# Optimization experiments

Hardware: AMD Instinct MI355X
Metric: run time of the kernel (lower is better)

## Reference

```python
import jax, jax.numpy as jnp
import numpy as np

BETA = 0.3        # SmoothL1Loss beta
LAMBDA_PHY = 0.15 # physics loss weight


def smooth_l1(d, beta):
    ad = jnp.abs(d)
    return jnp.where(ad < beta, 0.5 * d * d / beta, ad - 0.5 * beta)


def setup_inputs() -> dict:
    key = jax.random.key(0)
    k1, k2, k3, k4 = jax.random.split(key, 4)
    B, Z = 16384, 2048
    preds = jax.random.normal(k1, (B, Z, 1), dtype=jnp.float32)
    targets = jax.random.normal(k2, (B, Z), dtype=jnp.float32)
    current_temps = jax.random.normal(k3, (B, Z), dtype=jnp.float32)
    adjacency = jax.random.randint(k4, (Z, Z), 0, 2).astype(jnp.int32)
    return {"preds": preds, "targets": targets,
            "current_temps": current_temps, "adjacency": adjacency}


def reference(preds, targets, current_temps, adjacency):
    p = preds[:, :, 0]                               # [B, Z]
    num_zones = p.shape[1]
    pred_loss = smooth_l1(p - targets, BETA).mean()
    pred_change = p - current_temps                  # [B, Z]

    # Vectorized neighbor mean: replaces the per-zone Python loop with one
    # dense masked-adjacency contraction.
    mask = (adjacency > 0).astype(p.dtype)           # [Z, Z]
    deg = mask.sum(axis=1)                           # [Z]
    has_nb = deg > 0
    safe_deg = jnp.where(has_nb, deg, 1.0)
    avg_neighbor = jnp.einsum('zn,bn->bz', mask, current_temps) / safe_deg  # [B, Z]

    temp_diff = current_temps - avg_neighbor         # [B, Z]
    violation = jax.nn.softplus(temp_diff * pred_change)
    per_zone = violation.mean(axis=0)                # mean over batch, [Z]
    physics_loss = jnp.where(has_nb, per_zone, 0.0).sum() / num_zones

    total_loss = pred_loss + LAMBDA_PHY * physics_loss
    return (total_loss, physics_loss)
```

## Files before the change

kernel.cpp:

```cpp
#include <hip/hip_runtime.h>
#include <hip/hip_bf16.h>
#include <cmath>

#define BETA 0.3f
#define LAMBDA_PHY 0.15f

#define BM 128
#define BN 128
#define BKE 128
#define NT 256

typedef float f32x4 __attribute__((ext_vector_type(4)));
typedef int   i32x4 __attribute__((ext_vector_type(4)));
typedef int   i32x8 __attribute__((ext_vector_type(8)));

#define AS1 __attribute__((address_space(1)))
#define AS3 __attribute__((address_space(3)))

#define FENCE() asm volatile("" ::: "memory")
#define BARRIER() do { FENCE(); __builtin_amdgcn_s_barrier(); FENCE(); } while (0)
#define WAITV8() asm volatile("s_waitcnt vmcnt(8)" ::: "memory")
#define WAITV0() asm volatile("s_waitcnt vmcnt(0)" ::: "memory")

__device__ __forceinline__ float softplus_f(float x) {
    return fmaxf(x, 0.0f) + __logf(1.0f + __expf(-fabsf(x)));
}

__device__ __forceinline__ float smooth_l1_f(float d) {
    float ad = fabsf(d);
    return (ad < BETA) ? (0.5f / BETA) * d * d : (ad - 0.5f * BETA);
}

__device__ __forceinline__ unsigned f_e4m3(float f) {
    unsigned u = __builtin_bit_cast(unsigned, f);
    unsigned s = (u >> 24) & 0x80u;
    unsigned ab = u & 0x7fffffffu;
    float a = __builtin_bit_cast(float, ab);
    if (a >= 448.f) return s | 0x7Eu;
    if (a < 0.015625f) {
        int q = (int)rintf(a * 512.f);
        return s | (unsigned)q;
    }
    unsigned r = ab + 0x7FFFFu + ((ab >> 20) & 1u);
    unsigned ee = (r >> 23) - 120u;
    unsigned m = (r >> 20) & 7u;
    return s | (ee << 3) | m;
}

__global__ void k_prepconv(const int* __restrict__ adj, unsigned char* __restrict__ maskf8,
                           float* __restrict__ invdeg, float* __restrict__ hasnb, int Z,
                           const float* __restrict__ src, uint4* __restrict__ dst,
                           long n16, int ncb) {
    int t = threadIdx.x;
    if ((int)blockIdx.x < Z) {
        int z = blockIdx.x;
        const int* row = adj + (size_t)z * Z;
        unsigned char* mrow = maskf8 + (size_t)z * Z;
        int cnt = 0;
        for (int n = t; n < Z; n += blockDim.x) {
            int a = (row[n] > 0);
            mrow[n] = a ? (unsigned char)0x38 : (unsigned char)0;
            cnt += a;
        }
        for (int o = 32; o; o >>= 1) cnt += __shfl_down(cnt, o);
        __shared__ int rs[4];
        int lane = t & 63, wave = t >> 6;
        if (lane == 0) rs[wave] = cnt;
        __syncthreads();
        if (t == 0) {
            int deg = rs[0] + rs[1] + rs[2] + rs[3];
            invdeg[z] = (deg > 0) ? 1.0f / (float)deg : 1.0f;
            hasnb[z]  = (deg > 0) ? 1.0f : 0.0f;
        }
    } else {
        long i = (long)(blockIdx.x - Z) * blockDim.x + t;
        long stride = (long)ncb * blockDim.x;
        for (; i < n16; i += stride) {
            const float4* s = (const float4*)(src + i * 16);
            uint4 o;
            unsigned w[4];
#pragma unroll
            for (int q = 0; q < 4; ++q) {
                float4 v = s[q];
                w[q] = f_e4m3(v.x) | (f_e4m3(v.y) << 8) | (f_e4m3(v.z) << 16) | (f_e4m3(v.w) << 24);
            }
            o.x = w[0]; o.y = w[1]; o.z = w[2]; o.w = w[3];
            dst[i] = o;
        }
    }
}

__global__ __launch_bounds__(NT, 2) void k_gemm(
    const unsigned char* __restrict__ Af8,
    const unsigned char* __restrict__ Bf8,
    const float* __restrict__ preds,
    const float* __restrict__ targets,
    const float* __restrict__ ctemps,
    const float* __restrict__ invdeg,
    const float* __restrict__ hasnb,
    float* __restrict__ partials,
    int M, int N, int K)
{
    __shared__ __align__(16) unsigned char AsF[2 * BM * BKE];
    __shared__ __align__(16) unsigned char BsF[2 * BN * BKE];

    const int nwg = gridDim.x;
    const int ob = blockIdx.x;
    const int bid = (nwg % 8 == 0) ? ((ob % 8) * (nwg / 8) + ob / 8) : ob;
    const int ntiles = N / BN;
    const int mt = bid / ntiles;
    const int nt = bid % ntiles;
    const int row0 = mt * BM;
    const int col0 = nt * BN;
    const int t = threadIdx.x;
    const int lane = t & 63;
    const int wave = t >> 6;
    const int wm = wave >> 1;
    const int wn = wave & 1;
    const int fr = lane & 15;
    const int fq = lane >> 4;
    const int fr7 = fr & 7;

    const int tr = t >> 3;
    const int tc = t & 7;
    const int cs = tc ^ (tr & 7);

    int ofsA[2], ofsB[2];
#pragma unroll
    for (int p = 0; p < 2; ++p) {
        const int sp = (((fq + 4 * p) ^ fr7) << 4);
        ofsA[p] = (wm * 64 + fr) * BKE + sp;
        ofsB[p] = (wn * 64 + fr) * BKE + sp;
    }

    f32x4 acc[4][4];
#pragma unroll
    for (int m = 0; m < 4; ++m)
#pragma unroll
        for (int n = 0; n < 4; ++n)
            acc[m][n] = (f32x4){0.f, 0.f, 0.f, 0.f};

    const unsigned char* aSrc = Af8 + (size_t)(row0 + tr) * K + cs * 16;
    const unsigned char* bSrc = Bf8 + (size_t)(col0 + tr) * K + cs * 16;
    unsigned char* aDstC = &AsF[t * 16];
    unsigned char* bDstC = &BsF[t * 16];

#define STAGE(BUF) do {                                                                      \
    _Pragma("unroll")                                                                        \
    for (int r_ = 0; r_ < 4; ++r_)                                                           \
        __builtin_amdgcn_global_load_lds((const AS1 void*)(aSrc + (size_t)(r_ * 32) * K),    \
                                         (AS3 void*)(aDstC + (BUF) * 16384 + r_ * 4096), 16, 0, 0); \
    _Pragma("unroll")                                                                        \
    for (int r_ = 0; r_ < 4; ++r_)                                                           \
        __builtin_amdgcn_global_load_lds((const AS1 void*)(bSrc + (size_t)(r_ * 32) * K),    \
                                         (AS3 void*)(bDstC + (BUF) * 16384 + r_ * 4096), 16, 0, 0); \
    aSrc += BKE; bSrc += BKE;                                                                \
} while (0)

#define MFMA_TILE(BUF) do {                                                                  \
    i32x8 af_[4], bv_[4];                                                                    \
    _Pragma("unroll")                                                                        \
    for (int mi_ = 0; mi_ < 4; ++mi_) {                                                      \
        i32x4 lo_ = *(const i32x4*)(AsF + (BUF) * 16384 + ofsA[0] + mi_ * 2048);             \
        i32x4 hi_ = *(const i32x4*)(AsF + (BUF) * 16384 + ofsA[1] + mi_ * 2048);             \
        af_[mi_] = (i32x8){lo_[0], lo_[1], lo_[2], lo_[3], hi_[0], hi_[1], hi_[2], hi_[3]};  \
    }                                                                                        \
    _Pragma("unroll")                                                                        \
    for (int ni_ = 0; ni_ < 4; ++ni_) {                                                      \
        i32x4 lo_ = *(const i32x4*)(BsF + (BUF) * 16384 + ofsB[0] + ni_ * 2048);             \
        i32x4 hi_ = *(const i32x4*)(BsF + (BUF) * 16384 + ofsB[1] + ni_ * 2048);             \
        bv_[ni_] = (i32x8){lo_[0], lo_[1], lo_[2], lo_[3], hi_[0], hi_[1], hi_[2], hi_[3]};  \
    }                                                                                        \
    __builtin_amdgcn_s_setprio(1);                                                           \
    _Pragma("unroll")                                                                        \
    for (int mi_ = 0; mi_ < 4; ++mi_)                                                        \
    _Pragma("unroll")                                                                        \
    for (int ni_ = 0; ni_ < 4; ++ni_)                                                        \
        acc[mi_][ni_] = __builtin_amdgcn_mfma_scale_f32_16x16x128_f8f6f4(                    \
            af_[mi_], bv_[ni_], acc[mi_][ni_], 0, 0, 0, 0x7F, 0, 0x7F);                      \
    __builtin_amdgcn_s_setprio(0);                                                           \
} while (0)

    const int nk = K / BKE;
    const int nk2 = nk >> 1;
    STAGE(0);

    for (int i = 0; i < nk2; ++i) {
        STAGE(1);
        WAITV8();
        BARRIER();
        MFMA_TILE(0);
        BARRIER();
        if (i + 1 < nk2) {
            STAGE(0);
            WAITV8();
        } else {
            WAITV0();
        }
        BARRIER();
        MFMA_TILE(1);
        BARRIER();
    }

#undef STAGE
#undef MFMA_TILE

    const size_t rbase = (size_t)(row0 + wm * 64 + fq * 4) * N;
    const float* pB = preds   + rbase;
    const float* tB = targets + rbase;
    const float* cB = ctemps  + rbase;

    float vsum = 0.f, ssum = 0.f;
#pragma unroll
    for (int n = 0; n < 4; ++n) {
        const int z = col0 + wn * 64 + n * 16 + fr;
        const float idg = invdeg[z];
        const float hnb = hasnb[z];
#pragma unroll
        for (int mb = 0; mb < 2; ++mb) {
            float pv[8], tv[8], cf[8];
#pragma unroll
            for (int m2 = 0; m2 < 2; ++m2)
#pragma unroll
                for (int j = 0; j < 4; ++j) {
                    const size_t o = (size_t)((mb * 2 + m2) * 16 + j) * N + z;
                    pv[m2 * 4 + j] = pB[o];
                    tv[m2 * 4 + j] = tB[o];
                    cf[m2 * 4 + j] = cB[o];
                }
#pragma unroll
            for (int m2 = 0; m2 < 2; ++m2)
#pragma unroll
                for (int j = 0; j < 4; ++j) {
                    const int q = m2 * 4 + j;
                    float avg = acc[mb * 2 + m2][n][j] * idg;
                    float c = cf[q];
                    float p = pv[q];
                    float x = (c - avg) * (p - c);
                    vsum += softplus_f(x) * hnb;
                    ssum += smooth_l1_f(p - tv[q]);
                }
        }
    }
    for (int o = 32; o; o >>= 1) { vsum += __shfl_down(vsum, o); ssum += __shfl_down(ssum, o); }
    __shared__ float rv[4], rsm[4];
    if (lane == 0) { rv[wave] = vsum; rsm[wave] = ssum; }
    __syncthreads();
    if (t == 0) {
        partials[2 * (size_t)ob]     = rv[0] + rv[1] + rv[2] + rv[3];
        partials[2 * (size_t)ob + 1] = rsm[0] + rsm[1] + rsm[2] + rsm[3];
    }
}

__global__ void k_finalize(const float* __restrict__ partials, int nblk,
                           float* __restrict__ out, float invBZ) {
    __shared__ float sv[256], ss[256];
    int t = threadIdx.x;
    float v = 0.f, s = 0.f;
    for (int i = t; i < nblk; i += 256) { v += partials[2 * (size_t)i]; s += partials[2 * (size_t)i + 1]; }
    sv[t] = v; ss[t] = s;
    __syncthreads();
    for (int o = 128; o; o >>= 1) {
        if (t < o) { sv[t] += sv[t + o]; ss[t] += ss[t + o]; }
        __syncthreads();
    }
    if (t == 0) {
        float phys = sv[0] * invBZ;
        float pred = ss[0] * invBZ;
        out[0] = pred + LAMBDA_PHY * phys;
        out[1] = phys;
    }
}

__global__ void k_zero2(float* p) { if (threadIdx.x < 2) p[threadIdx.x] = 0.f; }

__global__ void k_fallback(const float* __restrict__ preds, const float* __restrict__ targets,
                           const float* __restrict__ ctemps, const int* __restrict__ adj,
                           float* __restrict__ acc2, int B, int Z) {
    extern __shared__ float crow[];
    int nzb = (Z + 255) / 256;
    int b = blockIdx.x / nzb;
    int zb = blockIdx.x % nzb;
    int t = threadIdx.x;
    const float* cr = ctemps + (size_t)b * Z;
    for (int n = t; n < Z; n += 256) crow[n] = cr[n];
    __syncthreads();
    int z = zb * 256 + t;
    float vsum = 0.f, ssum = 0.f;
    if (z < Z) {
        const int* arow = adj + (size_t)z * Z;
        float sum = 0.f; int deg = 0;
        for (int n = 0; n < Z; ++n) {
            if (arow[n] > 0) { sum += crow[n]; ++deg; }
        }
        float avg = (deg > 0) ? sum / (float)deg : 0.f;
        float c = crow[z];
        size_t idx = (size_t)b * Z + z;
        float p = preds[idx];
        float x = (c - avg) * (p - c);
        vsum = (deg > 0) ? softplus_f(x) : 0.f;
        ssum = smooth_l1_f(p - targets[idx]);
    }
    for (int o = 32; o; o >>= 1) { vsum += __shfl_down(vsum, o); ssum += __shfl_down(ssum, o); }
    __shared__ float rv[4], rs2[4];
    int lane = t & 63, wave = t >> 6;
    if (lane == 0) { rv[wave] = vsum; rs2[wave] = ssum; }
    __syncthreads();
    if (t == 0) {
        atomicAdd(&acc2[0], rv[0] + rv[1] + rv[2] + rv[3]);
        atomicAdd(&acc2[1], rs2[0] + rs2[1] + rs2[2] + rs2[3]);
    }
}

extern "C" void kernel_launch(void* const* d_in, const int* in_sizes, int n_in,
                              void* d_out, int out_size, void* d_ws, size_t ws_size,
                              hipStream_t stream) {
    const float* preds   = (const float*)d_in[0];
    const float* targets = (const float*)d_in[1];
    const float* ctemps  = (const float*)d_in[2];
    const int*   adj     = (const int*)d_in[3];
    float* out = (float*)d_out;

    long zz = in_sizes[3];
    int Z = (int)llround(sqrt((double)zz));
    int B = in_sizes[1] / Z;

    size_t off = 0;
    size_t maskOff = off; off += (size_t)Z * Z;
    size_t cf8Off  = off; off += (size_t)B * Z;
    size_t idgOff  = off; off += (size_t)Z * 4;
    size_t hnbOff  = off; off += (size_t)Z * 4;
    int nblk = (Z > 0 && B > 0 && (B % BM) == 0 && (Z % BN) == 0) ? (B / BM) * (Z / BN) : 0;
    size_t partOff = off; off += (size_t)(nblk > 0 ? nblk : 1) * 2 * 4;

    bool main_ok = (B % BM == 0) && (Z % BN == 0) && (Z % BKE == 0) &&
                   (((Z / BKE) % 2) == 0) && ((B * Z) % 16 == 0) && (ws_size >= off);

    float invBZ = (float)(1.0 / ((double)B * (double)Z));

    if (main_ok) {
        char* ws = (char*)d_ws;
        unsigned char* maskf8 = (unsigned char*)(ws + maskOff);
        unsigned char* cf8    = (unsigned char*)(ws + cf8Off);
        float* idg      = (float*)(ws + idgOff);
        float* hnb      = (float*)(ws + hnbOff);
        float* partials = (float*)(ws + partOff);

        long n16 = (long)B * Z / 16;
        int ncb = 2048;
        k_prepconv<<<Z + ncb, 256, 0, stream>>>(adj, maskf8, idg, hnb, Z,
                                                ctemps, (uint4*)cf8, n16, ncb);
        k_gemm<<<nblk, NT, 0, stream>>>(cf8, maskf8, preds, targets, ctemps, idg, hnb,
                                        partials, B, Z, Z);
        k_finalize<<<1, 256, 0, stream>>>(partials, nblk, out, invBZ);
    } else {
        float* acc2 = (float*)d_ws;
        k_zero2<<<1, 64, 0, stream>>>(acc2);
        int nzb = (Z + 255) / 256;
        k_fallback<<<B * nzb, 256, (size_t)Z * 4, stream>>>(preds, targets, ctemps, adj, acc2, B, Z);
        k_finalize<<<1, 256, 0, stream>>>(acc2, 1, out, invBZ);
    }
}
```

Before: 186.9 us.

## Shrink GEMM N-tile to 64 and load B fragments directly from global

The GEMM tile width drops from 128 to 64 columns, and the B operand's LDS staging buffer is removed. Each wave now loads its B fragments straight from global memory into registers once per K-step, and launch bounds are raised so more blocks can fit per CU. The aim is to cut LDS footprint and B staging overhead and get more occupancy for latency hiding. The cost is that the large A matrix is re-read twice as often across column tiles, so arithmetic intensity per tile drops, and the B register loads are not coalesced through LDS.

```diff
diff --git a/kernel.cpp b/kernel.cpp
--- a/kernel.cpp
+++ b/kernel.cpp
@@ -6,7 +6,7 @@
 #define LAMBDA_PHY 0.15f
 
 #define BM 128
-#define BN 128
+#define BN 64
 #define BKE 128
 #define NT 256
 
@@ -90,7 +90,7 @@
     }
 }
 
-__global__ __launch_bounds__(NT, 2) void k_gemm(
+__global__ __launch_bounds__(NT, 4) void k_gemm(
     const unsigned char* __restrict__ Af8,
     const unsigned char* __restrict__ Bf8,
     const float* __restrict__ preds,
@@ -102,7 +102,6 @@
     int M, int N, int K)
 {
     __shared__ __align__(16) unsigned char AsF[2 * BM * BKE];
-    __shared__ __align__(16) unsigned char BsF[2 * BN * BKE];
 
     const int nwg = gridDim.x;
     const int ob = blockIdx.x;
@@ -125,59 +124,57 @@
     const int tc = t & 7;
     const int cs = tc ^ (tr & 7);
 
-    int ofsA[2], ofsB[2];
-#pragma unroll
-    for (int p = 0; p < 2; ++p) {
-        const int sp = (((fq + 4 * p) ^ fr7) << 4);
-        ofsA[p] = (wm * 64 + fr) * BKE + sp;
-        ofsB[p] = (wn * 64 + fr) * BKE + sp;
-    }
-
-    f32x4 acc[4][4];
+    int ofsA[2];
+#pragma unroll
+    for (int p = 0; p < 2; ++p)
+        ofsA[p] = (wm * 64 + fr) * BKE + (((fq + 4 * p) ^ fr7) << 4);
+
+    f32x4 acc[4][2];
 #pragma unroll
     for (int m = 0; m < 4; ++m)
 #pragma unroll
-        for (int n = 0; n < 4; ++n)
+        for (int n = 0; n < 2; ++n)
             acc[m][n] = (f32x4){0.f, 0.f, 0.f, 0.f};
 
     const unsigned char* aSrc = Af8 + (size_t)(row0 + tr) * K + cs * 16;
-    const unsigned char* bSrc = Bf8 + (size_t)(col0 + tr) * K + cs * 16;
+    const unsigned char* bP0 = Bf8 + (size_t)(col0 + wn * 32 + fr) * K + fq * 16;
+    const unsigned char* bP1 = bP0 + (size_t)16 * K;
     unsigned char* aDstC = &AsF[t * 16];
-    unsigned char* bDstC = &BsF[t * 16];
 
 #define STAGE(BUF) do {                                                                      \
     _Pragma("unroll")                                                                        \
     for (int r_ = 0; r_ < 4; ++r_)                                                           \
         __builtin_amdgcn_global_load_lds((const AS1 void*)(aSrc + (size_t)(r_ * 32) * K),    \
                                          (AS3 void*)(aDstC + (BUF) * 16384 + r_ * 4096), 16, 0, 0); \
-    _Pragma("unroll")                                                                        \
-    for (int r_ = 0; r_ < 4; ++r_)                                                           \
-        __builtin_amdgcn_global_load_lds((const AS1 void*)(bSrc + (size_t)(r_ * 32) * K),    \
-                                         (AS3 void*)(bDstC + (BUF) * 16384 + r_ * 4096), 16, 0, 0); \
-    aSrc += BKE; bSrc += BKE;                                                                \
+    aSrc += BKE;                                                                             \
 } while (0)
 
-#define MFMA_TILE(BUF) do {                                                                  \
-    i32x8 af_[4], bv_[4];                                                                    \
+#define LOADB(BV0, BV1) do {                                                                 \
+    i32x4 b0_ = *(const i32x4*)(bP0);                                                        \
+    i32x4 b1_ = *(const i32x4*)(bP0 + 64);                                                   \
+    i32x4 c0_ = *(const i32x4*)(bP1);                                                        \
+    i32x4 c1_ = *(const i32x4*)(bP1 + 64);                                                   \
+    BV0 = (i32x8){b0_[0], b0_[1], b0_[2], b0_[3], b1_[0], b1_[1], b1_[2], b1_[3]};           \
+    BV1 = (i32x8){c0_[0], c0_[1], c0_[2], c0_[3], c1_[0], c1_[1], c1_[2], c1_[3]};           \
+    bP0 += BKE; bP1 += BKE;                                                                  \
+} while (0)
+
+#define MFMA_TILE(BUF, BV0, BV1) do {                                                        \
+    i32x8 af_[4];                                                                            \
     _Pragma("unroll")                                                                        \
     for (int mi_ = 0; mi_ < 4; ++mi_) {                                                      \
         i32x4 lo_ = *(const i32x4*)(AsF + (BUF) * 16384 + ofsA[0] + mi_ * 2048);             \
         i32x4 hi_ = *(const i32x4*)(AsF + (BUF) * 16384 + ofsA[1] + mi_ * 2048);             \
         af_[mi_] = (i32x8){lo_[0], lo_[1], lo_[2], lo_[3], hi_[0], hi_[1], hi_[2], hi_[3]};  \
     }                                                                                        \
-    _Pragma("unroll")                                                                        \
-    for (int ni_ = 0; ni_ < 4; ++ni_) {                                                      \
-        i32x4 lo_ = *(const i32x4*)(BsF + (BUF) * 16384 + ofsB[0] + ni_ * 2048);             \
-        i32x4 hi_ = *(const i32x4*)(BsF + (BUF) * 16384 + ofsB[1] + ni_ * 2048);             \
-        bv_[ni_] = (i32x8){lo_[0], lo_[1], lo_[2], lo_[3], hi_[0], hi_[1], hi_[2], hi_[3]};  \
-    }                                                                                        \
     __builtin_amdgcn_s_setprio(1);                                                           \
     _Pragma("unroll")                                                                        \
-    for (int mi_ = 0; mi_ < 4; ++mi_)                                                        \
-    _Pragma("unroll")                                                                        \
-    for (int ni_ = 0; ni_ < 4; ++ni_)                                                        \
-        acc[mi_][ni_] = __builtin_amdgcn_mfma_scale_f32_16x16x128_f8f6f4(                    \
-            af_[mi_], bv_[ni_], acc[mi_][ni_], 0, 0, 0, 0x7F, 0, 0x7F);                      \
+    for (int mi_ = 0; mi_ < 4; ++mi_) {                                                      \
+        acc[mi_][0] = __builtin_amdgcn_mfma_scale_f32_16x16x128_f8f6f4(                      \
+            af_[mi_], BV0, acc[mi_][0], 0, 0, 0, 0x7F, 0, 0x7F);                             \
+        acc[mi_][1] = __builtin_amdgcn_mfma_scale_f32_16x16x128_f8f6f4(                      \
+            af_[mi_], BV1, acc[mi_][1], 0, 0, 0, 0x7F, 0, 0x7F);                             \
+    }                                                                                        \
     __builtin_amdgcn_s_setprio(0);                                                           \
 } while (0)
 
@@ -186,11 +183,14 @@
     STAGE(0);
 
     for (int i = 0; i < nk2; ++i) {
+        i32x8 bv0, bv1;
+        LOADB(bv0, bv1);
         STAGE(1);
         WAITV8();
         BARRIER();
-        MFMA_TILE(0);
+        MFMA_TILE(0, bv0, bv1);
         BARRIER();
+        LOADB(bv0, bv1);
         if (i + 1 < nk2) {
             STAGE(0);
             WAITV8();
@@ -198,11 +198,12 @@
             WAITV0();
         }
         BARRIER();
-        MFMA_TILE(1);
+        MFMA_TILE(1, bv0, bv1);
         BARRIER();
     }
 
 #undef STAGE
+#undef LOADB
 #undef MFMA_TILE
 
     const size_t rbase = (size_t)(row0 + wm * 64 + fq * 4) * N;
@@ -212,8 +213,8 @@
 
     float vsum = 0.f, ssum = 0.f;
 #pragma unroll
-    for (int n = 0; n < 4; ++n) {
-        const int z = col0 + wn * 64 + n * 16 + fr;
+    for (int n = 0; n < 2; ++n) {
+        const int z = col0 + wn * 32 + n * 16 + fr;
         const float idg = invdeg[z];
         const float hnb = hasnb[z];
 #pragma unroll
```

Result: slower. 260.3 us (+39.3%).
